# Kernel tuning notes

Hardware: AMD Instinct MI355X
Metric: run time of the kernel (lower is better)

The kernel has to match this reference:

```python
import jax, jax.numpy as jnp
import numpy as np

N = 100000   # nodes
E = 3200000  # edges (avg degree 32)
IN = 128     # in_channels
H = 128      # hidden_channels
G = 512      # graphs in batch


def setup_inputs() -> dict:
    key = jax.random.key(0)
    ks = jax.random.split(key, 8)
    x = jax.random.normal(ks[0], (N, IN), dtype=jnp.float32)
    edge_index = jax.random.randint(ks[1], (2, E), 0, N, dtype=jnp.int64)
    batch = jnp.sort(jax.random.randint(ks[2], (N,), 0, G, dtype=jnp.int64))
    s_in = 1.0 / np.sqrt(IN)
    s_h = 1.0 / np.sqrt(H)
    W1 = jax.random.normal(ks[3], (IN, H), dtype=jnp.float32) * s_in
    b1 = jnp.zeros((H,), dtype=jnp.float32)
    W2 = jax.random.normal(ks[4], (H, H), dtype=jnp.float32) * s_h
    b2 = jnp.zeros((H,), dtype=jnp.float32)
    Wc = jax.random.normal(ks[5], (H, 1), dtype=jnp.float32) * s_h
    bc = jnp.zeros((1,), dtype=jnp.float32)
    return {"x": x, "edge_index": edge_index, "batch": batch,
            "W1": W1, "b1": b1, "W2": W2, "b2": b2, "Wc": Wc, "bc": bc}


def _gcn_conv(x, W, b, src, dst, n):
    # PyG GCNConv: x' = D^{-1/2} (A+I) D^{-1/2} X W + b  (self-loops already in src/dst)
    h = x @ W                                      # [n, H] small GEMM
    ones = jnp.ones(src.shape[0], dtype=h.dtype)
    deg = jax.ops.segment_sum(ones, dst, num_segments=n)
    dinv = jnp.where(deg > 0, jax.lax.rsqrt(deg), 0.0)
    norm = dinv[src] * dinv[dst]                   # [E+n]
    msgs = h[src] * norm[:, None]                  # gather + scale (memory-bound)
    return jax.ops.segment_sum(msgs, dst, num_segments=n) + b


def reference(x, edge_index, batch, W1, b1, W2, b2, Wc, bc):
    n = x.shape[0]
    loop = jnp.arange(n, dtype=edge_index.dtype)
    src = jnp.concatenate([edge_index[0], loop])   # add self-loops
    dst = jnp.concatenate([edge_index[1], loop])
    h = jax.nn.relu(_gcn_conv(x, W1, b1, src, dst, n))
    h = jax.nn.relu(_gcn_conv(h, W2, b2, src, dst, n))
    # global_mean_pool: segment mean over graph ids
    counts = jax.ops.segment_sum(jnp.ones(n, dtype=h.dtype), batch, num_segments=G)
    sums = jax.ops.segment_sum(h, batch, num_segments=G)
    pooled = sums / jnp.maximum(counts, 1.0)[:, None]   # [G, H]
    return jax.nn.sigmoid(pooled @ Wc + bc)             # [G, 1]
```

## Files before the change

kernel.cpp:

```cpp
#include <hip/hip_runtime.h>

typedef unsigned short ushort_t;
typedef unsigned int uint_t;
typedef unsigned char u8_t;

typedef __bf16 bf16x8 __attribute__((ext_vector_type(8)));
typedef float f32x4 __attribute__((ext_vector_type(4)));
typedef uint_t uint32x4 __attribute__((ext_vector_type(4)));
typedef uint_t uint32x2 __attribute__((ext_vector_type(2)));
typedef _Float16 h2 __attribute__((ext_vector_type(2)));

#define EPB 20480
#define NSH 7
#define CAP 6144

__device__ __forceinline__ float b2f(ushort_t u) {
    union { uint_t ui; float f; } c; c.ui = ((uint_t)u) << 16; return c.f;
}
__device__ __forceinline__ ushort_t f2b(float f) {
    union { float f; uint_t ui; } c; c.f = f;
    uint_t u = c.ui;
    uint_t r = (u + 0x7fffu + ((u >> 16) & 1u)) >> 16;
    return (ushort_t)r;
}
__device__ __forceinline__ u8_t f2e5(float x) {
    ushort_t h = __builtin_bit_cast(ushort_t, (_Float16)x);
    uint_t r = ((uint_t)h + 0x7Fu + ((h >> 8) & 1u)) >> 8;
    return (u8_t)r;
}
__device__ __forceinline__ void upk_add(uint_t d, h2* acc) {
    uint_t A = __builtin_amdgcn_perm(0u, d, 0x010C000Cu);
    uint_t B = __builtin_amdgcn_perm(0u, d, 0x030C020Cu);
    acc[0] += __builtin_bit_cast(h2, A);
    acc[1] += __builtin_bit_cast(h2, B);
}

__global__ __launch_bounds__(256) void p1_hist(const int* __restrict__ dst,
                                               int* __restrict__ H,
                                               const float* __restrict__ W1,
                                               const float* __restrict__ W2,
                                               ushort_t* __restrict__ W1t,
                                               ushort_t* __restrict__ W2t,
                                               u8_t* __restrict__ h8z,
                                               int E, int NBLK, int B, int N) {
    int t = threadIdx.x, c = blockIdx.x;
    if (c >= NBLK + 128) {
        if (t < 32) ((uint_t*)h8z)[(size_t)N * 32 + t] = 0u;
        return;
    }
    if (c >= NBLK) {
        int idx = (c - NBLK) * 256 + t;
        int sel = idx >> 14;
        int i = idx & 16383;
        int k = i >> 7, nn = i & 127;
        const float* S = sel ? W2 : W1;
        ushort_t* D = sel ? W2t : W1t;
        D[nn * 128 + k] = f2b(S[k * 128 + nn]);
        return;
    }
    __shared__ int hist[1024];
    for (int b = t; b < 1024; b += 256) hist[b] = 0;
    __syncthreads();
    int base = c * EPB;
    int lim = min(E - base, EPB);
    for (int i = t; i < lim; i += 256)
        atomicAdd(&hist[dst[base + i] >> NSH], 1);
    __syncthreads();
    for (int b = t; b < B; b += 256) H[b * NBLK + c] = hist[b];
}

__global__ __launch_bounds__(256) void reduce256(const int* __restrict__ in,
                                                 int* __restrict__ bsums, int n) {
    __shared__ int s[256];
    int t = threadIdx.x, g = blockIdx.x * 256 + t;
    s[t] = (g < n) ? in[g] : 0;
    __syncthreads();
    for (int o = 128; o > 0; o >>= 1) {
        if (t < o) s[t] += s[t + o];
        __syncthreads();
    }
    if (t == 0) bsums[blockIdx.x] = s[0];
}

__global__ __launch_bounds__(512) void scan_small(const int* __restrict__ in,
                                                  int* __restrict__ outEx, int n) {
    __shared__ int s[512];
    int t = threadIdx.x;
    int v = (t < n) ? in[t] : 0;
    s[t] = v;
    __syncthreads();
    for (int o = 1; o < 512; o <<= 1) {
        int x = 0;
        if (t >= o) x = s[t - o];
        __syncthreads();
        s[t] += x;
        __syncthreads();
    }
    if (t < n) outEx[t] = s[t] - v;
}

__global__ __launch_bounds__(256) void scan256ex(const int* __restrict__ in,
                                                 const int* __restrict__ boffs,
                                                 int* __restrict__ outEx, int n) {
    __shared__ int s[256];
    int t = threadIdx.x, g = blockIdx.x * 256 + t;
    int v = (g < n) ? in[g] : 0;
    s[t] = v;
    __syncthreads();
    for (int o = 1; o < 256; o <<= 1) {
        int x = 0;
        if (t >= o) x = s[t - o];
        __syncthreads();
        s[t] += x;
        __syncthreads();
    }
    if (g < n) outEx[g] = boffs[blockIdx.x] + s[t] - v;
}

__global__ __launch_bounds__(256) void p3_scatter(const int* __restrict__ src,
                                                  const int* __restrict__ dst,
                                                  const int* __restrict__ Hex,
                                                  uint_t* __restrict__ packed,
                                                  int E, int NBLK, int B) {
    __shared__ int offsL[1024];
    __shared__ int cur[1024];
    int t = threadIdx.x, c = blockIdx.x;
    for (int b = t; b < B; b += 256) {
        offsL[b] = Hex[b * NBLK + c];
        cur[b] = 0;
    }
    __syncthreads();
    int base = c * EPB;
    int lim = min(E - base, EPB);
    for (int i = t; i < lim; i += 256) {
        int d = dst[base + i];
        int s = src[base + i];
        int b = d >> NSH;
        int r = atomicAdd(&cur[b], 1);
        packed[offsL[b] + r] = ((uint_t)s << NSH) | (uint_t)(d & 127);
    }
}

__global__ __launch_bounds__(256) void p4_build(const uint_t* __restrict__ packed,
                                                const int* __restrict__ Hex,
                                                int* __restrict__ adj,
                                                int* __restrict__ offs,
                                                float* __restrict__ dinv,
                                                int E, int N, int NBLK, int B) {
    __shared__ uint_t ebuf[CAP];
    __shared__ uint_t sbuf[CAP];
    __shared__ int hist[1024];
    __shared__ int hbase[1024];
    __shared__ int psum[256];
    __shared__ int dcnt[128], loc[128], cur[128];
    int t = threadIdx.x, b = blockIdx.x;
    int bs = Hex[b * NBLK];
    int be = (b + 1 < B) ? Hex[(b + 1) * NBLK] : E;
    int m = be - bs;
    for (int i = t; i < 1024; i += 256) hist[i] = 0;
    if (t < 128) dcnt[t] = 0;
    __syncthreads();
    bool fits = (m <= CAP);
    for (int i = t; i < m; i += 256) {
        uint_t p = packed[bs + i];
        if (fits) ebuf[i] = p;
        atomicAdd(&dcnt[p & 127], 1);
        atomicAdd(&hist[p >> (2 * NSH)], 1);
    }
    __syncthreads();
    int v0 = hist[4 * t], v1 = hist[4 * t + 1], v2 = hist[4 * t + 2], v3 = hist[4 * t + 3];
    int tot = v0 + v1 + v2 + v3;
    psum[t] = tot;
    __syncthreads();
    for (int o = 1; o < 256; o <<= 1) {
        int x = 0;
        if (t >= o) x = psum[t - o];
        __syncthreads();
        psum[t] += x;
        __syncthreads();
    }
    int base = psum[t] - tot;
    hbase[4 * t]     = base;
    hbase[4 * t + 1] = base + v0;
    hbase[4 * t + 2] = base + v0 + v1;
    hbase[4 * t + 3] = base + v0 + v1 + v2;
    if (t < 128) loc[t] = dcnt[t];
    __syncthreads();
    for (int o = 1; o < 128; o <<= 1) {
        int x = 0;
        if (t < 128 && t >= o) x = loc[t - o];
        __syncthreads();
        if (t < 128) loc[t] += x;
        __syncthreads();
    }
    if (t < 128) {
        int ex = loc[t] - dcnt[t];
        int node = b * 128 + t;
        if (node < N) {
            offs[node] = bs + ex;
            dinv[node] = rsqrtf((float)(dcnt[t] + 1));
        }
        loc[t] = ex;
        cur[t] = 0;
    }
    if (b == B - 1 && t == 0) offs[N] = E;
    __syncthreads();
    if (fits) {
        for (int i = t; i < m; i += 256) {
            uint_t p = ebuf[i];
            int r = atomicAdd(&hbase[p >> (2 * NSH)], 1);
            sbuf[r] = p;
        }
        __syncthreads();
        for (int i = t; i < m; i += 256) {
            uint_t p = sbuf[i];
            int l = p & 127;
            int r = atomicAdd(&cur[l], 1);
            adj[bs + loc[l] + r] = (int)(p >> NSH);
        }
    } else {
        for (int i = t; i < m; i += 256) {
            uint_t p = packed[bs + i];
            int l = p & 127;
            int r = atomicAdd(&cur[l], 1);
            adj[bs + loc[l] + r] = (int)(p >> NSH);
        }
    }
}

__global__ __launch_bounds__(256, 4) void gemm_scale(const ushort_t* __restrict__ Xin,
                                                     const ushort_t* __restrict__ Wt,
                                                     const float* __restrict__ dinv,
                                                     u8_t* __restrict__ Hout8, int n) {
    __shared__ ushort_t lds[128 * 136];
    int tid = threadIdx.x;
    for (int i = tid; i < 128 * 16; i += 256) {
        int r = i >> 4, c8 = (i & 15) << 3;
        *(uint32x4*)(lds + r * 136 + c8) = *(const uint32x4*)(Wt + r * 128 + c8);
    }
    __syncthreads();
    int lane = tid & 63, wave = tid >> 6;
    int m = lane & 15, q = lane >> 4;
    int row0 = blockIdx.x * 64 + wave * 16;
    int ar = row0 + m;
    if (ar > n - 1) ar = n - 1;
    bf16x8 a[4];
#pragma unroll
    for (int ks = 0; ks < 4; ++ks)
        a[ks] = __builtin_bit_cast(bf16x8,
            *(const uint32x4*)(Xin + (size_t)ar * 128 + ks * 32 + q * 8));
    f32x4 acc[8];
    f32x4 zero = {0.f, 0.f, 0.f, 0.f};
#pragma unroll
    for (int nt = 0; nt < 8; ++nt) acc[nt] = zero;
#pragma unroll
    for (int nt = 0; nt < 8; ++nt) {
#pragma unroll
        for (int ks = 0; ks < 4; ++ks) {
            bf16x8 b = __builtin_bit_cast(bf16x8,
                *(const uint32x4*)(lds + (nt * 16 + m) * 136 + ks * 32 + q * 8));
            acc[nt] = __builtin_amdgcn_mfma_f32_16x16x32_bf16(a[ks], b, acc[nt], 0, 0, 0);
        }
    }
    float dv[4];
#pragma unroll
    for (int r = 0; r < 4; ++r) {
        int gr = row0 + q * 4 + r;
        dv[r] = (gr < n) ? dinv[gr] : 0.f;
    }
#pragma unroll
    for (int nt = 0; nt < 8; ++nt) {
#pragma unroll
        for (int r = 0; r < 4; ++r) {
            int gr = row0 + q * 4 + r;
            if (gr < n)
                Hout8[(size_t)gr * 128 + nt * 16 + m] = f2e5(acc[nt][r] * dv[r]);
        }
    }
}

__global__ __launch_bounds__(256, 4) void gemm_scale_f32(const float* __restrict__ Xf,
                                                         const ushort_t* __restrict__ Wt,
                                                         const float* __restrict__ dinv,
                                                         u8_t* __restrict__ Hout8, int n) {
    __shared__ ushort_t lds[128 * 136];
    int tid = threadIdx.x;
    for (int i = tid; i < 128 * 16; i += 256) {
        int r = i >> 4, c8 = (i & 15) << 3;
        *(uint32x4*)(lds + r * 136 + c8) = *(const uint32x4*)(Wt + r * 128 + c8);
    }
    __syncthreads();
    int lane = tid & 63, wave = tid >> 6;
    int m = lane & 15, q = lane >> 4;
    int row0 = blockIdx.x * 64 + wave * 16;
    int ar = row0 + m;
    if (ar > n - 1) ar = n - 1;
    bf16x8 a[4];
#pragma unroll
    for (int ks = 0; ks < 4; ++ks) {
        const float* p = Xf + (size_t)ar * 128 + ks * 32 + q * 8;
        f32x4 lo = *(const f32x4*)p;
        f32x4 hi = *(const f32x4*)(p + 4);
        ushort_t t[8];
        t[0] = f2b(lo[0]); t[1] = f2b(lo[1]); t[2] = f2b(lo[2]); t[3] = f2b(lo[3]);
        t[4] = f2b(hi[0]); t[5] = f2b(hi[1]); t[6] = f2b(hi[2]); t[7] = f2b(hi[3]);
        a[ks] = __builtin_bit_cast(bf16x8, *(uint32x4*)t);
    }
    f32x4 acc[8];
    f32x4 zero = {0.f, 0.f, 0.f, 0.f};
#pragma unroll
    for (int nt = 0; nt < 8; ++nt) acc[nt] = zero;
#pragma unroll
    for (int nt = 0; nt < 8; ++nt) {
#pragma unroll
        for (int ks = 0; ks < 4; ++ks) {
            bf16x8 b = __builtin_bit_cast(bf16x8,
                *(const uint32x4*)(lds + (nt * 16 + m) * 136 + ks * 32 + q * 8));
            acc[nt] = __builtin_amdgcn_mfma_f32_16x16x32_bf16(a[ks], b, acc[nt], 0, 0, 0);
        }
    }
    float dv[4];
#pragma unroll
    for (int r = 0; r < 4; ++r) {
        int gr = row0 + q * 4 + r;
        dv[r] = (gr < n) ? dinv[gr] : 0.f;
    }
#pragma unroll
    for (int nt = 0; nt < 8; ++nt) {
#pragma unroll
        for (int r = 0; r < 4; ++r) {
            int gr = row0 + q * 4 + r;
            if (gr < n)
                Hout8[(size_t)gr * 128 + nt * 16 + m] = f2e5(acc[nt][r] * dv[r]);
        }
    }
}

__device__ __forceinline__ void agg_body16(const u8_t* base8, const int* __restrict__ adj,
                                           int beg, int end, int g, int nz, h2* acc) {
    if (beg >= end) return;
    int endm1 = end - 1;
    for (int e = beg; e < end; e += 40) {
        int s[5];
#pragma unroll
        for (int j = 0; j < 5; ++j) {
            int idx0 = e + 8 * j + g;
            int idx = idx0 < endm1 ? idx0 : endm1;
            int sv = adj[idx];
            s[j] = (idx0 < end) ? sv : nz;
        }
        __builtin_amdgcn_sched_barrier(0);
        uint32x4 w[5];
#pragma unroll
        for (int j = 0; j < 5; ++j)
            w[j] = *(const uint32x4*)(base8 + (size_t)s[j] * 128);
        __builtin_amdgcn_sched_barrier(0);
#pragma unroll
        for (int j = 0; j < 5; ++j) {
            upk_add(w[j][0], acc);
            upk_add(w[j][1], acc + 2);
            upk_add(w[j][2], acc + 4);
            upk_add(w[j][3], acc + 6);
        }
    }
}

__global__ __launch_bounds__(256, 4) void agg_kernel(const u8_t* __restrict__ Hs8,
                                                     const int* __restrict__ adj,
                                                     const int* __restrict__ offs,
                                                     const float* __restrict__ dinv,
                                                     const float* __restrict__ bias,
                                                     ushort_t* __restrict__ Out, int n) {
    int node = blockIdx.x * 4 + (threadIdx.x >> 6);
    if (node >= n) return;
    int lane = threadIdx.x & 63;
    int g = lane >> 3;
    int l8 = lane & 7;
    int col = l8 * 16;
    const u8_t* base8 = Hs8 + col;
    const int beg = offs[node], end = offs[node + 1];
    h2 acc[8];
    h2 hz = {(_Float16)0.f, (_Float16)0.f};
#pragma unroll
    for (int k = 0; k < 8; ++k) acc[k] = hz;
    if (g == 0) {
        uint32x4 w = *(const uint32x4*)(base8 + (size_t)node * 128);
        upk_add(w[0], acc);
        upk_add(w[1], acc + 2);
        upk_add(w[2], acc + 4);
        upk_add(w[3], acc + 6);
    }
    agg_body16(base8, adj, beg, end, g, n, acc);
#pragma unroll
    for (int k = 0; k < 8; ++k) {
        uint_t v = __builtin_bit_cast(uint_t, acc[k]);
        acc[k] += __builtin_bit_cast(h2, (uint_t)__shfl_xor(v, 8, 64));
        v = __builtin_bit_cast(uint_t, acc[k]);
        acc[k] += __builtin_bit_cast(h2, (uint_t)__shfl_xor(v, 16, 64));
        v = __builtin_bit_cast(uint_t, acc[k]);
        acc[k] += __builtin_bit_cast(h2, (uint_t)__shfl_xor(v, 32, 64));
    }
    if (g == 0) {
        float di = dinv[node];
        ushort_t o[16];
#pragma unroll
        for (int k = 0; k < 8; ++k) {
            float f0 = (float)acc[k][0];
            float f1 = (float)acc[k][1];
            o[2 * k]     = f2b(fmaxf(di * f0 + bias[col + 2 * k], 0.f));
            o[2 * k + 1] = f2b(fmaxf(di * f1 + bias[col + 2 * k + 1], 0.f));
        }
        *(uint32x4*)(Out + (size_t)node * 128 + col)     = *(uint32x4*)o;
        *(uint32x4*)(Out + (size_t)node * 128 + col + 8) = *(uint32x4*)(o + 8);
    }
}

__global__ __launch_bounds__(256, 4) void agg_pool_kernel(const u8_t* __restrict__ Hs8,
                                                          const int* __restrict__ adj,
                                                          const int* __restrict__ offs,
                                                          const float* __restrict__ dinv,
                                                          const float* __restrict__ bias,
                                                          const float* __restrict__ Wc,
                                                          float* __restrict__ Sout, int n) {
    int node = blockIdx.x * 4 + (threadIdx.x >> 6);
    if (node >= n) return;
    int lane = threadIdx.x & 63;
    int g = lane >> 3;
    int l8 = lane & 7;
    int col = l8 * 16;
    const u8_t* base8 = Hs8 + col;
    const int beg = offs[node], end = offs[node + 1];
    h2 acc[8];
    h2 hz = {(_Float16)0.f, (_Float16)0.f};
#pragma unroll
    for (int k = 0; k < 8; ++k) acc[k] = hz;
    if (g == 0) {
        uint32x4 w = *(const uint32x4*)(base8 + (size_t)node * 128);
        upk_add(w[0], acc);
        upk_add(w[1], acc + 2);
        upk_add(w[2], acc + 4);
        upk_add(w[3], acc + 6);
    }
    agg_body16(base8, adj, beg, end, g, n, acc);
#pragma unroll
    for (int k = 0; k < 8; ++k) {
        uint_t v = __builtin_bit_cast(uint_t, acc[k]);
        acc[k] += __builtin_bit_cast(h2, (uint_t)__shfl_xor(v, 8, 64));
        v = __builtin_bit_cast(uint_t, acc[k]);
        acc[k] += __builtin_bit_cast(h2, (uint_t)__shfl_xor(v, 16, 64));
        v = __builtin_bit_cast(uint_t, acc[k]);
        acc[k] += __builtin_bit_cast(h2, (uint_t)__shfl_xor(v, 32, 64));
    }
    float local = 0.f;
    float di = dinv[node];
#pragma unroll
    for (int k = 0; k < 8; ++k) {
        float f0 = fmaxf(di * (float)acc[k][0] + bias[col + 2 * k], 0.f);
        float f1 = fmaxf(di * (float)acc[k][1] + bias[col + 2 * k + 1], 0.f);
        local += f0 * Wc[col + 2 * k] + f1 * Wc[col + 2 * k + 1];
    }
    local += __shfl_xor(local, 1, 64);
    local += __shfl_xor(local, 2, 64);
    local += __shfl_xor(local, 4, 64);
    if (lane == 0) Sout[node] = local;
}

__global__ __launch_bounds__(256) void pool2_kernel(const float* __restrict__ S,
                                                    const int* __restrict__ batch,
                                                    const float* __restrict__ bc,
                                                    float* __restrict__ out, int n) {
    int g = blockIdx.x;
    int t = threadIdx.x;
    int lo = 0, hi = n;
    while (lo < hi) { int mid = (lo + hi) >> 1; if (batch[mid] < g) lo = mid + 1; else hi = mid; }
    int start = lo;
    hi = n;
    while (lo < hi) { int mid = (lo + hi) >> 1; if (batch[mid] < g + 1) lo = mid + 1; else hi = mid; }
    int stop = lo;
    float s = 0.f;
    for (int i = start + t; i < stop; i += 256) s += S[i];
    __shared__ float red[256];
    red[t] = s;
    __syncthreads();
    for (int o = 128; o > 0; o >>= 1) {
        if (t < o) red[t] += red[t + o];
        __syncthreads();
    }
    if (t == 0) {
        int cg = stop - start;
        float z = red[0] / (float)(cg > 0 ? cg : 1) + bc[0];
        out[g] = 1.f / (1.f + expf(-z));
    }
}

extern "C" void kernel_launch(void* const* d_in, const int* in_sizes, int n_in,
                              void* d_out, int out_size, void* d_ws, size_t ws_size,
                              hipStream_t stream) {
    const float* X     = (const float*)d_in[0];
    const int* ei      = (const int*)d_in[1];
    const int* batch   = (const int*)d_in[2];
    const float* W1    = (const float*)d_in[3];
    const float* b1    = (const float*)d_in[4];
    const float* W2    = (const float*)d_in[5];
    const float* b2    = (const float*)d_in[6];
    const float* Wc    = (const float*)d_in[7];
    const float* bc    = (const float*)d_in[8];

    const int N = in_sizes[2];
    const int E = in_sizes[1] / 2;
    const int G = out_size;
    const int* srcv = ei;
    const int* dstv = ei + E;

    const int NBLK = (E + EPB - 1) / EPB;
    const int B    = (N + 127) >> NSH;
    const int n0   = B * NBLK;
    const int g1   = (n0 + 255) / 256;

    char* p = (char*)d_ws;
    auto alloc = [&](size_t bytes) -> void* {
        void* r = (void*)p;
        p += (bytes + 255) & ~(size_t)255;
        return r;
    };
    int* H         = (int*)alloc((size_t)n0 * 4);
    int* Hex       = (int*)alloc((size_t)n0 * 4);
    int* S1        = (int*)alloc((size_t)g1 * 4);
    int* S1ex      = (int*)alloc((size_t)g1 * 4);
    uint_t* packed = (uint_t*)alloc((size_t)E * 4);
    int* adj       = (int*)alloc((size_t)E * 4);
    int* offs      = (int*)alloc(((size_t)N + 1) * 4);
    float* dinv    = (float*)alloc((size_t)N * 4);
    ushort_t* W1t  = (ushort_t*)alloc(16384 * 2);
    ushort_t* W2t  = (ushort_t*)alloc(16384 * 2);
    u8_t* h8       = (u8_t*)alloc(((size_t)N + 1) * 128);
    ushort_t* bufA = (ushort_t*)alloc((size_t)N * 128 * 2);
    float* Snode   = (float*)alloc((size_t)N * 4);

    p1_hist<<<NBLK + 129, 256, 0, stream>>>(dstv, H, W1, W2, W1t, W2t, h8, E, NBLK, B, N);
    reduce256<<<g1, 256, 0, stream>>>(H, S1, n0);
    scan_small<<<1, 512, 0, stream>>>(S1, S1ex, g1);
    scan256ex<<<g1, 256, 0, stream>>>(H, S1ex, Hex, n0);
    p3_scatter<<<NBLK, 256, 0, stream>>>(srcv, dstv, Hex, packed, E, NBLK, B);
    p4_build<<<B, 256, 0, stream>>>(packed, Hex, adj, offs, dinv, E, N, NBLK, B);

    const int GB = (N + 63) / 64;
    const int AB = (N + 3) / 4;
    gemm_scale_f32<<<GB, 256, 0, stream>>>(X, W1t, dinv, h8, N);
    agg_kernel<<<AB, 256, 0, stream>>>(h8, adj, offs, dinv, b1, bufA, N);
    gemm_scale<<<GB, 256, 0, stream>>>(bufA, W2t, dinv, h8, N);
    agg_pool_kernel<<<AB, 256, 0, stream>>>(h8, adj, offs, dinv, b2, Wc, Snode, N);
    pool2_kernel<<<G, 256, 0, stream>>>(Snode, batch, bc, (float*)d_out, N);
}
```

Baseline: 378.4 us.

## Pad CSR adjacency rows to multiples of eight with self-loop and dummy entries

```diff
diff --git a/kernel.cpp b/kernel.cpp
--- a/kernel.cpp
+++ b/kernel.cpp
@@ -13,6 +13,7 @@
 #define EPB 20480
 #define NSH 7
 #define CAP 6144
+#define BPAD 904
 
 __device__ __forceinline__ float b2f(ushort_t u) {
     union { uint_t ui; float f; } c; c.ui = ((uint_t)u) << 16; return c.f;
@@ -145,6 +146,7 @@
                                                 const int* __restrict__ Hex,
                                                 int* __restrict__ adj,
                                                 int* __restrict__ offs,
+                                                int* __restrict__ dgr,
                                                 float* __restrict__ dinv,
                                                 int E, int N, int NBLK, int B) {
     __shared__ uint_t ebuf[CAP];
@@ -153,6 +155,7 @@
     __shared__ int hbase[1024];
     __shared__ int psum[256];
     __shared__ int dcnt[128], loc[128], cur[128];
+    __shared__ int pdg[128], ploc[128];
     int t = threadIdx.x, b = blockIdx.x;
     int bs = Hex[b * NBLK];
     int be = (b + 1 < B) ? Hex[(b + 1) * NBLK] : E;
@@ -184,26 +187,35 @@
     hbase[4 * t + 1] = base + v0;
     hbase[4 * t + 2] = base + v0 + v1;
     hbase[4 * t + 3] = base + v0 + v1 + v2;
-    if (t < 128) loc[t] = dcnt[t];
+    if (t < 128) {
+        int pd = (dcnt[t] + 8) & ~7;
+        pdg[t] = pd;
+        ploc[t] = pd;
+    }
     __syncthreads();
     for (int o = 1; o < 128; o <<= 1) {
         int x = 0;
-        if (t < 128 && t >= o) x = loc[t - o];
-        __syncthreads();
-        if (t < 128) loc[t] += x;
-        __syncthreads();
-    }
+        if (t < 128 && t >= o) x = ploc[t - o];
+        __syncthreads();
+        if (t < 128) ploc[t] += x;
+        __syncthreads();
+    }
+    int bsp = ((bs + 7) & ~7) + b * BPAD;
     if (t < 128) {
-        int ex = loc[t] - dcnt[t];
+        int ex = ploc[t] - pdg[t];
         int node = b * 128 + t;
         if (node < N) {
-            offs[node] = bs + ex;
+            int nbase = bsp + ex;
+            offs[node] = nbase;
+            dgr[node]  = pdg[t];
             dinv[node] = rsqrtf((float)(dcnt[t] + 1));
-        }
-        loc[t] = ex;
+            adj[nbase] = node;
+            for (int i = dcnt[t] + 1; i < pdg[t]; ++i)
+                adj[nbase + i] = N;
+        }
+        loc[t] = ex + 1;
         cur[t] = 0;
     }
-    if (b == B - 1 && t == 0) offs[N] = E;
     __syncthreads();
     if (fits) {
         for (int i = t; i < m; i += 256) {
@@ -216,14 +228,14 @@
             uint_t p = sbuf[i];
             int l = p & 127;
             int r = atomicAdd(&cur[l], 1);
-            adj[bs + loc[l] + r] = (int)(p >> NSH);
+            adj[bsp + loc[l] + r] = (int)(p >> NSH);
         }
     } else {
         for (int i = t; i < m; i += 256) {
             uint_t p = packed[bs + i];
             int l = p & 127;
             int r = atomicAdd(&cur[l], 1);
-            adj[bs + loc[l] + r] = (int)(p >> NSH);
+            adj[bsp + loc[l] + r] = (int)(p >> NSH);
         }
     }
 }
@@ -336,88 +348,94 @@
     }
 }
 
-__device__ __forceinline__ void agg_body16(const u8_t* base8, const int* __restrict__ adj,
-                                           int beg, int end, int g, int nz, h2* acc) {
-    if (beg >= end) return;
-    int endm1 = end - 1;
-    for (int e = beg; e < end; e += 40) {
-        int s[5];
-#pragma unroll
-        for (int j = 0; j < 5; ++j) {
-            int idx0 = e + 8 * j + g;
-            int idx = idx0 < endm1 ? idx0 : endm1;
-            int sv = adj[idx];
-            s[j] = (idx0 < end) ? sv : nz;
-        }
-        __builtin_amdgcn_sched_barrier(0);
-        uint32x4 w[5];
-#pragma unroll
-        for (int j = 0; j < 5; ++j)
-            w[j] = *(const uint32x4*)(base8 + (size_t)s[j] * 128);
-        __builtin_amdgcn_sched_barrier(0);
-#pragma unroll
-        for (int j = 0; j < 5; ++j) {
-            upk_add(w[j][0], acc);
-            upk_add(w[j][1], acc + 2);
-            upk_add(w[j][2], acc + 4);
-            upk_add(w[j][3], acc + 6);
-        }
+__device__ __forceinline__ void agg_core(const u8_t* __restrict__ Hs8,
+                                         const int* __restrict__ adj,
+                                         int beg, int pd, int g, uint_t colb,
+                                         int nz, h2* acc) {
+    for (int e = 0; e < pd; e += 32) {
+        const int4 sv = *(const int4*)(adj + beg + e + g * 4);
+        bool ok = (e + g * 4) < pd;
+        int s0 = ok ? sv.x : nz;
+        int s1 = ok ? sv.y : nz;
+        int s2 = ok ? sv.z : nz;
+        int s3 = ok ? sv.w : nz;
+        uint_t o0 = ((uint_t)s0 << 7) | colb;
+        uint_t o1 = ((uint_t)s1 << 7) | colb;
+        uint_t o2 = ((uint_t)s2 << 7) | colb;
+        uint_t o3 = ((uint_t)s3 << 7) | colb;
+        uint32x4 w0 = *(const uint32x4*)(Hs8 + o0);
+        uint32x4 w1 = *(const uint32x4*)(Hs8 + o1);
+        uint32x4 w2 = *(const uint32x4*)(Hs8 + o2);
+        uint32x4 w3 = *(const uint32x4*)(Hs8 + o3);
+        upk_add(w0[0], acc); upk_add(w0[1], acc + 2);
+        upk_add(w0[2], acc + 4); upk_add(w0[3], acc + 6);
+        upk_add(w1[0], acc); upk_add(w1[1], acc + 2);
+        upk_add(w1[2], acc + 4); upk_add(w1[3], acc + 6);
+        upk_add(w2[0], acc); upk_add(w2[1], acc + 2);
+        upk_add(w2[2], acc + 4); upk_add(w2[3], acc + 6);
+        upk_add(w3[0], acc); upk_add(w3[1], acc + 2);
+        upk_add(w3[2], acc + 4); upk_add(w3[3], acc + 6);
+    }
+}
+
+__device__ __forceinline__ void slot_reduce(h2* acc) {
+#pragma unroll
+    for (int k = 0; k < 8; ++k) {
+        uint_t v = __builtin_bit_cast(uint_t, acc[k]);
+        acc[k] += __builtin_bit_cast(h2, (uint_t)__shfl_xor(v, 1, 64));
+        v = __builtin_bit_cast(uint_t, acc[k]);
+        acc[k] += __builtin_bit_cast(h2, (uint_t)__shfl_xor(v, 2, 64));
+        v = __builtin_bit_cast(uint_t, acc[k]);
+        acc[k] += __builtin_bit_cast(h2, (uint_t)__shfl_xor(v, 4, 64));
     }
 }
 
 __global__ __launch_bounds__(256, 4) void agg_kernel(const u8_t* __restrict__ Hs8,
                                                      const int* __restrict__ adj,
                                                      const int* __restrict__ offs,
+                                                     const int* __restrict__ dgr,
                                                      const float* __restrict__ dinv,
                                                      const float* __restrict__ bias,
                                                      ushort_t* __restrict__ Out, int n) {
     int node = blockIdx.x * 4 + (threadIdx.x >> 6);
     if (node >= n) return;
     int lane = threadIdx.x & 63;
-    int g = lane >> 3;
-    int l8 = lane & 7;
-    int col = l8 * 16;
-    const u8_t* base8 = Hs8 + col;
-    const int beg = offs[node], end = offs[node + 1];
+    int g = lane & 7;
+    int c = lane >> 3;
+    uint_t colb = (uint_t)c * 16;
+    const int beg = offs[node];
+    const int pd  = dgr[node];
     h2 acc[8];
     h2 hz = {(_Float16)0.f, (_Float16)0.f};
 #pragma unroll
     for (int k = 0; k < 8; ++k) acc[k] = hz;
-    if (g == 0) {
-        uint32x4 w = *(const uint32x4*)(base8 + (size_t)node * 128);
-        upk_add(w[0], acc);
-        upk_add(w[1], acc + 2);
-        upk_add(w[2], acc + 4);
-        upk_add(w[3], acc + 6);
-    }
-    agg_body16(base8, adj, beg, end, g, n, acc);
-#pragma unroll
-    for (int k = 0; k < 8; ++k) {
-        uint_t v = __builtin_bit_cast(uint_t, acc[k]);
-        acc[k] += __builtin_bit_cast(h2, (uint_t)__shfl_xor(v, 8, 64));
-        v = __builtin_bit_cast(uint_t, acc[k]);
-        acc[k] += __builtin_bit_cast(h2, (uint_t)__shfl_xor(v, 16, 64));
-        v = __builtin_bit_cast(uint_t, acc[k]);
-        acc[k] += __builtin_bit_cast(h2, (uint_t)__shfl_xor(v, 32, 64));
-    }
+    agg_core(Hs8, adj, beg, pd, g, colb, n, acc);
+    slot_reduce(acc);
     if (g == 0) {
         float di = dinv[node];
+        float bv[16];
+        const f32x4* bp = (const f32x4*)(bias + colb);
+        *(f32x4*)(bv)      = bp[0];
+        *(f32x4*)(bv + 4)  = bp[1];
+        *(f32x4*)(bv + 8)  = bp[2];
+        *(f32x4*)(bv + 12) = bp[3];
         ushort_t o[16];
 #pragma unroll
         for (int k = 0; k < 8; ++k) {
             float f0 = (float)acc[k][0];
             float f1 = (float)acc[k][1];
-            o[2 * k]     = f2b(fmaxf(di * f0 + bias[col + 2 * k], 0.f));
-            o[2 * k + 1] = f2b(fmaxf(di * f1 + bias[col + 2 * k + 1], 0.f));
-        }
-        *(uint32x4*)(Out + (size_t)node * 128 + col)     = *(uint32x4*)o;
-        *(uint32x4*)(Out + (size_t)node * 128 + col + 8) = *(uint32x4*)(o + 8);
+            o[2 * k]     = f2b(fmaxf(di * f0 + bv[2 * k], 0.f));
+            o[2 * k + 1] = f2b(fmaxf(di * f1 + bv[2 * k + 1], 0.f));
+        }
+        *(uint32x4*)(Out + (size_t)node * 128 + colb)     = *(uint32x4*)o;
+        *(uint32x4*)(Out + (size_t)node * 128 + colb + 8) = *(uint32x4*)(o + 8);
     }
 }
 
 __global__ __launch_bounds__(256, 4) void agg_pool_kernel(const u8_t* __restrict__ Hs8,
                                                           const int* __restrict__ adj,
                                                           const int* __restrict__ offs,
+                                                          const int* __restrict__ dgr,
                                                           const float* __restrict__ dinv,
                                                           const float* __restrict__ bias,
                                                           const float* __restrict__ Wc,
@@ -425,43 +443,35 @@
     int node = blockIdx.x * 4 + (threadIdx.x >> 6);
     if (node >= n) return;
     int lane = threadIdx.x & 63;
-    int g = lane >> 3;
-    int l8 = lane & 7;
-    int col = l8 * 16;
-    const u8_t* base8 = Hs8 + col;
-    const int beg = offs[node], end = offs[node + 1];
+    int g = lane & 7;
+    int c = lane >> 3;
+    uint_t colb = (uint_t)c * 16;
+    const int beg = offs[node];
+    const int pd  = dgr[node];
     h2 acc[8];
     h2 hz = {(_Float16)0.f, (_Float16)0.f};
 #pragma unroll
     for (int k = 0; k < 8; ++k) acc[k] = hz;
-    if (g == 0) {
-        uint32x4 w = *(const uint32x4*)(base8 + (size_t)node * 128);
-        upk_add(w[0], acc);
-        upk_add(w[1], acc + 2);
-        upk_add(w[2], acc + 4);
-        upk_add(w[3], acc + 6);
-    }
-    agg_body16(base8, adj, beg, end, g, n, acc);
+    agg_core(Hs8, adj, beg, pd, g, colb, n, acc);
+    slot_reduce(acc);
+    float di = dinv[node];
+    float bv[16], wv[16];
+    const f32x4* bp = (const f32x4*)(bias + colb);
+    const f32x4* wp = (const f32x4*)(Wc + colb);
+    *(f32x4*)(bv) = bp[0]; *(f32x4*)(bv + 4) = bp[1];
+    *(f32x4*)(bv + 8) = bp[2]; *(f32x4*)(bv + 12) = bp[3];
+    *(f32x4*)(wv) = wp[0]; *(f32x4*)(wv + 4) = wp[1];
+    *(f32x4*)(wv + 8) = wp[2]; *(f32x4*)(wv + 12) = wp[3];
+    float local = 0.f;
 #pragma unroll
     for (int k = 0; k < 8; ++k) {
-        uint_t v = __builtin_bit_cast(uint_t, acc[k]);
-        acc[k] += __builtin_bit_cast(h2, (uint_t)__shfl_xor(v, 8, 64));
-        v = __builtin_bit_cast(uint_t, acc[k]);
-        acc[k] += __builtin_bit_cast(h2, (uint_t)__shfl_xor(v, 16, 64));
-        v = __builtin_bit_cast(uint_t, acc[k]);
-        acc[k] += __builtin_bit_cast(h2, (uint_t)__shfl_xor(v, 32, 64));
-    }
-    float local = 0.f;
-    float di = dinv[node];
-#pragma unroll
-    for (int k = 0; k < 8; ++k) {
-        float f0 = fmaxf(di * (float)acc[k][0] + bias[col + 2 * k], 0.f);
-        float f1 = fmaxf(di * (float)acc[k][1] + bias[col + 2 * k + 1], 0.f);
-        local += f0 * Wc[col + 2 * k] + f1 * Wc[col + 2 * k + 1];
-    }
-    local += __shfl_xor(local, 1, 64);
-    local += __shfl_xor(local, 2, 64);
-    local += __shfl_xor(local, 4, 64);
+        float f0 = fmaxf(di * (float)acc[k][0] + bv[2 * k], 0.f);
+        float f1 = fmaxf(di * (float)acc[k][1] + bv[2 * k + 1], 0.f);
+        local += f0 * wv[2 * k] + f1 * wv[2 * k + 1];
+    }
+    local += __shfl_xor(local, 8, 64);
+    local += __shfl_xor(local, 16, 64);
+    local += __shfl_xor(local, 32, 64);
     if (lane == 0) Sout[node] = local;
 }
 
@@ -528,8 +538,9 @@
     int* S1        = (int*)alloc((size_t)g1 * 4);
     int* S1ex      = (int*)alloc((size_t)g1 * 4);
     uint_t* packed = (uint_t*)alloc((size_t)E * 4);
-    int* adj       = (int*)alloc((size_t)E * 4);
+    int* adj       = (int*)alloc(((size_t)E + (size_t)B * BPAD + 128) * 4);
     int* offs      = (int*)alloc(((size_t)N + 1) * 4);
+    int* dgr       = (int*)alloc((size_t)N * 4);
     float* dinv    = (float*)alloc((size_t)N * 4);
     ushort_t* W1t  = (ushort_t*)alloc(16384 * 2);
     ushort_t* W2t  = (ushort_t*)alloc(16384 * 2);
@@ -542,13 +553,13 @@
     scan_small<<<1, 512, 0, stream>>>(S1, S1ex, g1);
     scan256ex<<<g1, 256, 0, stream>>>(H, S1ex, Hex, n0);
     p3_scatter<<<NBLK, 256, 0, stream>>>(srcv, dstv, Hex, packed, E, NBLK, B);
-    p4_build<<<B, 256, 0, stream>>>(packed, Hex, adj, offs, dinv, E, N, NBLK, B);
+    p4_build<<<B, 256, 0, stream>>>(packed, Hex, adj, offs, dgr, dinv, E, N, NBLK, B);
 
     const int GB = (N + 63) / 64;
     const int AB = (N + 3) / 4;
     gemm_scale_f32<<<GB, 256, 0, stream>>>(X, W1t, dinv, h8, N);
-    agg_kernel<<<AB, 256, 0, stream>>>(h8, adj, offs, dinv, b1, bufA, N);
+    agg_kernel<<<AB, 256, 0, stream>>>(h8, adj, offs, dgr, dinv, b1, bufA, N);
     gemm_scale<<<GB, 256, 0, stream>>>(bufA, W2t, dinv, h8, N);
-    agg_pool_kernel<<<AB, 256, 0, stream>>>(h8, adj, offs, dinv, b2, Wc, Snode, N);
+    agg_pool_kernel<<<AB, 256, 0, stream>>>(h8, adj, offs, dgr, dinv, b2, Wc, Snode, N);
     pool2_kernel<<<G, 256, 0, stream>>>(Snode, batch, bc, (float*)d_out, N);
 }
```

After: 415.9 us. +9.9%, slower.
